# Performance work log

Hardware: AMD Instinct MI355X
Metric: run time of the kernel (lower is better)

The kernel has to match this reference:

```python
import jax, jax.numpy as jnp
import numpy as np

N, E = 100000, 1600000
IN_C, HID_C, OUT_C = 128, 32, 16


def setup_inputs() -> dict:
    key = jax.random.key(0)
    k1, k2, k3, k4, k5, k6 = jax.random.split(key, 6)
    x = jax.random.normal(k1, (N, IN_C), dtype=jnp.float32)
    edge_index = jax.random.randint(k2, (2, E), 0, N, dtype=jnp.int64)
    # glorot-style init for GCN weights
    W1 = jax.random.normal(k3, (IN_C, HID_C), dtype=jnp.float32) * (1.0 / np.sqrt(IN_C))
    b1 = jnp.zeros((HID_C,), dtype=jnp.float32)
    W2 = jax.random.normal(k4, (HID_C, OUT_C), dtype=jnp.float32) * (1.0 / np.sqrt(HID_C))
    b2 = jnp.zeros((OUT_C,), dtype=jnp.float32)
    return {"x": x, "edge_index": edge_index, "W1": W1, "b1": b1, "W2": W2, "b2": b2}


def _gcn_conv(x, W, b, src, dst, norm, n_nodes):
    # linear transform first (PyG GCNConv order), then normalized scatter-add
    h = x @ W                                  # [N, C_out]
    msg = h[src] * norm[:, None]               # gather + per-edge scale
    agg = jax.ops.segment_sum(msg, dst, num_segments=n_nodes)  # scatter-add
    return agg + b


def reference(x, edge_index, W1, b1, W2, b2):
    n_nodes = x.shape[0]
    loop = jnp.arange(n_nodes, dtype=edge_index.dtype)
    # add self-loops (PyG default add_self_loops=True)
    src = jnp.concatenate([edge_index[0], loop])
    dst = jnp.concatenate([edge_index[1], loop])
    # symmetric normalization: deg computed on graph WITH self-loops
    deg = jax.ops.segment_sum(jnp.ones_like(dst, dtype=x.dtype), dst, num_segments=n_nodes)
    dinv = jnp.where(deg > 0, jax.lax.rsqrt(deg), 0.0)
    norm = dinv[src] * dinv[dst]               # [E + N]

    h = _gcn_conv(x, W1, b1, src, dst, norm, n_nodes)
    h = jax.nn.relu(h)
    out = _gcn_conv(h, W2, b2, src, dst, norm, n_nodes)
    return out
```

## Files before the change

kernel.cpp:

```cpp
#include <hip/hip_runtime.h>
#include <stdint.h>


#define TPB 256

__global__ void k_zero2(unsigned int* __restrict__ a, unsigned int* __restrict__ b, int n) {
    int i = blockIdx.x * blockDim.x + threadIdx.x;
    if (i < n) { a[i] = 0u; b[i] = 0u; }
}

__global__ void k_count(const int* __restrict__ dst, unsigned int* __restrict__ cnt, int E) {
    int stride = gridDim.x * blockDim.x;
    for (int i = blockIdx.x * blockDim.x + threadIdx.x; i < E; i += stride)
        atomicAdd(&cnt[(unsigned int)dst[i]], 1u);
}

__global__ void k_dinv(const unsigned int* __restrict__ cnt, float* __restrict__ dinv, int n) {
    int i = blockIdx.x * blockDim.x + threadIdx.x;
    if (i < n) dinv[i] = rsqrtf(1.0f + (float)cnt[i]);
}

__global__ void k_blocksums(const unsigned int* __restrict__ cnt, unsigned int* __restrict__ partial, int n) {
    __shared__ unsigned int sm[TPB];
    int i = blockIdx.x * TPB + threadIdx.x;
    sm[threadIdx.x] = (i < n) ? cnt[i] : 0u;
    __syncthreads();
    for (int off = TPB / 2; off > 0; off >>= 1) {
        if (threadIdx.x < off) sm[threadIdx.x] += sm[threadIdx.x + off];
        __syncthreads();
    }
    if (threadIdx.x == 0) partial[blockIdx.x] = sm[0];
}

__global__ void k_scanpartials(unsigned int* __restrict__ partial, int nb) {
    __shared__ unsigned int sm[512];
    int t = threadIdx.x;
    unsigned int v = (t < nb) ? partial[t] : 0u;
    sm[t] = v;
    __syncthreads();
    for (int off = 1; off < 512; off <<= 1) {
        unsigned int add = (t >= off) ? sm[t - off] : 0u;
        __syncthreads();
        sm[t] += add;
        __syncthreads();
    }
    if (t < nb) partial[t] = sm[t] - v;
}

__global__ void k_rowptr(const unsigned int* __restrict__ cnt, const unsigned int* __restrict__ partial,
                         unsigned int* __restrict__ rowptr, int n, int E) {
    __shared__ unsigned int sm[TPB];
    int t = threadIdx.x;
    int i = blockIdx.x * TPB + t;
    unsigned int v = (i < n) ? cnt[i] : 0u;
    sm[t] = v;
    __syncthreads();
    for (int off = 1; off < TPB; off <<= 1) {
        unsigned int add = (t >= off) ? sm[t - off] : 0u;
        __syncthreads();
        sm[t] += add;
        __syncthreads();
    }
    if (i < n) rowptr[i] = partial[blockIdx.x] + sm[t] - v;
    if (i == n - 1) rowptr[n] = (unsigned int)E;
}

__global__ void k_fill(const int* __restrict__ ei, const float* __restrict__ dinv,
                       const unsigned int* __restrict__ rowptr, unsigned int* __restrict__ cursor,
                       int2* __restrict__ adj, int E) {
    const int* srcp = ei;
    const int* dstp = ei + E;
    int stride = gridDim.x * blockDim.x;
    for (int i = blockIdx.x * blockDim.x + threadIdx.x; i < E; i += stride) {
        int s = srcp[i], d = dstp[i];
        unsigned int pos = rowptr[d] + atomicAdd(&cursor[d], 1u);
        adj[pos] = make_int2(s, __float_as_int(dinv[s] * dinv[d]));
    }
}

__global__ void k_gemm1(const float* __restrict__ x, const float* __restrict__ W1,
                        float* __restrict__ h1, int n) {
    int t = blockIdx.x * blockDim.x + threadIdx.x;
    if (t >= n * 32) return;
    int row = t >> 5, j = t & 31;
    const float4* xr = (const float4*)(x + (size_t)row * 128);
    float acc = 0.f;
#pragma unroll 8
    for (int k4 = 0; k4 < 32; ++k4) {
        float4 xv = xr[k4];
        int k = k4 * 4;
        acc = fmaf(xv.x, W1[(k + 0) * 32 + j], acc);
        acc = fmaf(xv.y, W1[(k + 1) * 32 + j], acc);
        acc = fmaf(xv.z, W1[(k + 2) * 32 + j], acc);
        acc = fmaf(xv.w, W1[(k + 3) * 32 + j], acc);
    }
    h1[t] = acc;
}

__global__ void k_agg1(const float* __restrict__ h1, const float* __restrict__ dinv,
                       const unsigned int* __restrict__ rowptr, const int2* __restrict__ adj,
                       float* __restrict__ agg1, int n) {
    int t = blockIdx.x * blockDim.x + threadIdx.x;
    if (t >= n * 8) return;
    int node = t >> 3, c4 = (t & 7) * 4;
    float di = dinv[node];
    float di2 = di * di;
    float4 acc = *(const float4*)(h1 + (size_t)node * 32 + c4);
    acc.x *= di2; acc.y *= di2; acc.z *= di2; acc.w *= di2;
    unsigned int e1 = rowptr[node + 1];
    for (unsigned int e = rowptr[node]; e < e1; ++e) {
        int2 a = adj[e];
        float nrm = __int_as_float(a.y);
        float4 hv = *(const float4*)(h1 + (size_t)a.x * 32 + c4);
        acc.x = fmaf(hv.x, nrm, acc.x);
        acc.y = fmaf(hv.y, nrm, acc.y);
        acc.z = fmaf(hv.z, nrm, acc.z);
        acc.w = fmaf(hv.w, nrm, acc.w);
    }
    *(float4*)(agg1 + (size_t)node * 32 + c4) = acc;
}

__global__ void k_gemm2(const float* __restrict__ agg1, const float* __restrict__ b1,
                        const float* __restrict__ W2, float* __restrict__ h2, int n) {
    int t = blockIdx.x * blockDim.x + threadIdx.x;
    if (t >= n * 16) return;
    int row = t >> 4, j = t & 15;
    const float4* ar = (const float4*)(agg1 + (size_t)row * 32);
    float acc = 0.f;
#pragma unroll
    for (int k4 = 0; k4 < 8; ++k4) {
        float4 av = ar[k4];
        int k = k4 * 4;
        float v0 = fmaxf(av.x + b1[k + 0], 0.f);
        float v1 = fmaxf(av.y + b1[k + 1], 0.f);
        float v2 = fmaxf(av.z + b1[k + 2], 0.f);
        float v3 = fmaxf(av.w + b1[k + 3], 0.f);
        acc = fmaf(v0, W2[(k + 0) * 16 + j], acc);
        acc = fmaf(v1, W2[(k + 1) * 16 + j], acc);
        acc = fmaf(v2, W2[(k + 2) * 16 + j], acc);
        acc = fmaf(v3, W2[(k + 3) * 16 + j], acc);
    }
    h2[t] = acc;
}

__global__ void k_agg2(const float* __restrict__ h2, const float* __restrict__ dinv,
                       const float* __restrict__ b2,
                       const unsigned int* __restrict__ rowptr, const int2* __restrict__ adj,
                       float* __restrict__ out, int n) {
    int t = blockIdx.x * blockDim.x + threadIdx.x;
    if (t >= n * 4) return;
    int node = t >> 2, c4 = (t & 3) * 4;
    float di = dinv[node];
    float di2 = di * di;
    float4 hv0 = *(const float4*)(h2 + (size_t)node * 16 + c4);
    float4 bv = *(const float4*)(b2 + c4);
    float4 acc = make_float4(fmaf(hv0.x, di2, bv.x), fmaf(hv0.y, di2, bv.y),
                             fmaf(hv0.z, di2, bv.z), fmaf(hv0.w, di2, bv.w));
    unsigned int e1 = rowptr[node + 1];
    for (unsigned int e = rowptr[node]; e < e1; ++e) {
        int2 a = adj[e];
        float nrm = __int_as_float(a.y);
        float4 hv = *(const float4*)(h2 + (size_t)a.x * 16 + c4);
        acc.x = fmaf(hv.x, nrm, acc.x);
        acc.y = fmaf(hv.y, nrm, acc.y);
        acc.z = fmaf(hv.z, nrm, acc.z);
        acc.w = fmaf(hv.w, nrm, acc.w);
    }
    *(float4*)(out + (size_t)node * 16 + c4) = acc;
}

static inline char* align256(char* p) {
    return (char*)(((uintptr_t)p + 255) & ~(uintptr_t)255);
}

extern "C" void kernel_launch(void* const* d_in, const int* in_sizes, int n_in,
                              void* d_out, int out_size, void* d_ws, size_t ws_size,
                              hipStream_t stream) {
    const float* x  = (const float*)d_in[0];
    const int*   ei = (const int*)d_in[1];
    const float* W1 = (const float*)d_in[2];
    const float* b1 = (const float*)d_in[3];
    const float* W2 = (const float*)d_in[4];
    const float* b2 = (const float*)d_in[5];
    float*       out = (float*)d_out;

    int N = in_sizes[0] / 128;
    int E = in_sizes[1] / 2;

    char* p = (char*)d_ws;
    unsigned int* rowptr  = (unsigned int*)p;  p = align256(p + (size_t)(N + 1) * 4);
    unsigned int* cnt     = (unsigned int*)p;  p = align256(p + (size_t)N * 4);
    unsigned int* cursor  = (unsigned int*)p;  p = align256(p + (size_t)N * 4);
    unsigned int* partial = (unsigned int*)p;  p = align256(p + 512 * 4);
    float*        dinv    = (float*)p;         p = align256(p + (size_t)N * 4);
    int2*         adj     = (int2*)p;          p = align256(p + (size_t)E * 8);
    float*        h1      = (float*)p;         p = align256(p + (size_t)N * 32 * 4);
    float*        agg1    = (float*)p;
    float*        h2      = h1;

    int gN = (N + TPB - 1) / TPB;
    int NB = gN;

    k_zero2        <<<gN,   TPB, 0, stream>>>(cnt, cursor, N);
    k_count        <<<2048, TPB, 0, stream>>>(ei + E, cnt, E);
    k_dinv         <<<gN,   TPB, 0, stream>>>(cnt, dinv, N);
    k_blocksums    <<<NB,   TPB, 0, stream>>>(cnt, partial, N);
    k_scanpartials <<<1,    512, 0, stream>>>(partial, NB);
    k_rowptr       <<<NB,   TPB, 0, stream>>>(cnt, partial, rowptr, N, E);
    k_fill         <<<2048, TPB, 0, stream>>>(ei, dinv, rowptr, cursor, adj, E);

    k_gemm1 <<<(N * 32 + TPB - 1) / TPB, TPB, 0, stream>>>(x, W1, h1, N);
    k_agg1  <<<(N * 8  + TPB - 1) / TPB, TPB, 0, stream>>>(h1, dinv, rowptr, adj, agg1, N);
    k_gemm2 <<<(N * 16 + TPB - 1) / TPB, TPB, 0, stream>>>(agg1, b1, W2, h2, N);
    k_agg2  <<<(N * 4  + TPB - 1) / TPB, TPB, 0, stream>>>(h2, dinv, b2, rowptr, adj, out, N);
}
```

Before: 418.6 us.

## Tile both dense GEMMs through shared memory with register blocking

Rewrites the two node-feature GEMMs so each block stages a tile of input rows and a transposed, padded copy of the weight matrix in shared memory. Each thread then computes eight output rows, reusing one weight vector across them. The goal is to replace redundant per-thread global loads of x and W with coalesced tile loads and LDS reuse. In exchange the kernels use more shared memory per block (about 49 KB for gemm1) and more accumulator registers, which may lower occupancy.

After: 358.5 us. -14.4%, faster.

```diff
diff --git a/kernel.cpp b/kernel.cpp
--- a/kernel.cpp
+++ b/kernel.cpp
@@ -78,23 +78,49 @@
     }
 }
 
-__global__ void k_gemm1(const float* __restrict__ x, const float* __restrict__ W1,
-                        float* __restrict__ h1, int n) {
-    int t = blockIdx.x * blockDim.x + threadIdx.x;
-    if (t >= n * 32) return;
-    int row = t >> 5, j = t & 31;
-    const float4* xr = (const float4*)(x + (size_t)row * 128);
-    float acc = 0.f;
-#pragma unroll 8
+__global__ __launch_bounds__(TPB) void k_gemm1(const float* __restrict__ x, const float* __restrict__ W1,
+                                               float* __restrict__ h1, int n) {
+    __shared__ float4 smx4[64 * 32];
+    __shared__ float4 smw4[32 * 33];
+    float* smw = (float*)smw4;
+    int t = threadIdx.x;
+    int row0 = blockIdx.x * 64;
+
+#pragma unroll
+    for (int it = 0; it < 16; ++it) {
+        int idx = it * TPB + t;
+        int k = idx >> 5, j = idx & 31;
+        smw[j * 132 + k] = W1[idx];
+    }
+    const float4* x4 = (const float4*)x;
+    int lim = n * 32;
+#pragma unroll
+    for (int it = 0; it < 8; ++it) {
+        int fo = it * TPB + t;
+        int gi = row0 * 32 + fo;
+        smx4[fo] = (gi < lim) ? x4[gi] : make_float4(0.f, 0.f, 0.f, 0.f);
+    }
+    __syncthreads();
+
+    int j = t & 31, rb = (t >> 5) * 8;
+    float acc[8] = {0.f, 0.f, 0.f, 0.f, 0.f, 0.f, 0.f, 0.f};
+#pragma unroll 4
     for (int k4 = 0; k4 < 32; ++k4) {
-        float4 xv = xr[k4];
-        int k = k4 * 4;
-        acc = fmaf(xv.x, W1[(k + 0) * 32 + j], acc);
-        acc = fmaf(xv.y, W1[(k + 1) * 32 + j], acc);
-        acc = fmaf(xv.z, W1[(k + 2) * 32 + j], acc);
-        acc = fmaf(xv.w, W1[(k + 3) * 32 + j], acc);
-    }
-    h1[t] = acc;
+        float4 wv = smw4[j * 33 + k4];
+#pragma unroll
+        for (int i = 0; i < 8; ++i) {
+            float4 xv = smx4[(rb + i) * 32 + k4];
+            acc[i] = fmaf(xv.x, wv.x, acc[i]);
+            acc[i] = fmaf(xv.y, wv.y, acc[i]);
+            acc[i] = fmaf(xv.z, wv.z, acc[i]);
+            acc[i] = fmaf(xv.w, wv.w, acc[i]);
+        }
+    }
+#pragma unroll
+    for (int i = 0; i < 8; ++i) {
+        int row = row0 + rb + i;
+        if (row < n) h1[(size_t)row * 32 + j] = acc[i];
+    }
 }
 
 __global__ void k_agg1(const float* __restrict__ h1, const float* __restrict__ dinv,
@@ -120,27 +146,56 @@
     *(float4*)(agg1 + (size_t)node * 32 + c4) = acc;
 }
 
-__global__ void k_gemm2(const float* __restrict__ agg1, const float* __restrict__ b1,
-                        const float* __restrict__ W2, float* __restrict__ h2, int n) {
-    int t = blockIdx.x * blockDim.x + threadIdx.x;
-    if (t >= n * 16) return;
-    int row = t >> 4, j = t & 15;
-    const float4* ar = (const float4*)(agg1 + (size_t)row * 32);
-    float acc = 0.f;
+__global__ __launch_bounds__(TPB) void k_gemm2(const float* __restrict__ agg1, const float* __restrict__ b1,
+                                               const float* __restrict__ W2, float* __restrict__ h2, int n) {
+    __shared__ float4 sma4[128 * 8];
+    __shared__ float4 smw24[16 * 9];
+    float* smw2 = (float*)smw24;
+    int t = threadIdx.x;
+    int row0 = blockIdx.x * 128;
+
+#pragma unroll
+    for (int it = 0; it < 2; ++it) {
+        int idx = it * TPB + t;
+        int k = idx >> 4, j = idx & 15;
+        smw2[j * 36 + k] = W2[idx];
+    }
+    const float4* a4 = (const float4*)agg1;
+    const float4* b14 = (const float4*)b1;
+    int lim = n * 8;
+#pragma unroll
+    for (int it = 0; it < 4; ++it) {
+        int fo = it * TPB + t;
+        int gi = row0 * 8 + fo;
+        float4 v = (gi < lim) ? a4[gi] : make_float4(0.f, 0.f, 0.f, 0.f);
+        float4 b = b14[fo & 7];
+        v.x = fmaxf(v.x + b.x, 0.f);
+        v.y = fmaxf(v.y + b.y, 0.f);
+        v.z = fmaxf(v.z + b.z, 0.f);
+        v.w = fmaxf(v.w + b.w, 0.f);
+        sma4[fo] = v;
+    }
+    __syncthreads();
+
+    int j = t & 15, rb = (t >> 4) * 8;
+    float acc[8] = {0.f, 0.f, 0.f, 0.f, 0.f, 0.f, 0.f, 0.f};
 #pragma unroll
     for (int k4 = 0; k4 < 8; ++k4) {
-        float4 av = ar[k4];
-        int k = k4 * 4;
-        float v0 = fmaxf(av.x + b1[k + 0], 0.f);
-        float v1 = fmaxf(av.y + b1[k + 1], 0.f);
-        float v2 = fmaxf(av.z + b1[k + 2], 0.f);
-        float v3 = fmaxf(av.w + b1[k + 3], 0.f);
-        acc = fmaf(v0, W2[(k + 0) * 16 + j], acc);
-        acc = fmaf(v1, W2[(k + 1) * 16 + j], acc);
-        acc = fmaf(v2, W2[(k + 2) * 16 + j], acc);
-        acc = fmaf(v3, W2[(k + 3) * 16 + j], acc);
-    }
-    h2[t] = acc;
+        float4 wv = smw24[j * 9 + k4];
+#pragma unroll
+        for (int i = 0; i < 8; ++i) {
+            float4 xv = sma4[(rb + i) * 8 + k4];
+            acc[i] = fmaf(xv.x, wv.x, acc[i]);
+            acc[i] = fmaf(xv.y, wv.y, acc[i]);
+            acc[i] = fmaf(xv.z, wv.z, acc[i]);
+            acc[i] = fmaf(xv.w, wv.w, acc[i]);
+        }
+    }
+#pragma unroll
+    for (int i = 0; i < 8; ++i) {
+        int row = row0 + rb + i;
+        if (row < n) h2[(size_t)row * 16 + j] = acc[i];
+    }
 }
 
 __global__ void k_agg2(const float* __restrict__ h2, const float* __restrict__ dinv,
@@ -209,8 +264,8 @@
     k_rowptr       <<<NB,   TPB, 0, stream>>>(cnt, partial, rowptr, N, E);
     k_fill         <<<2048, TPB, 0, stream>>>(ei, dinv, rowptr, cursor, adj, E);
 
-    k_gemm1 <<<(N * 32 + TPB - 1) / TPB, TPB, 0, stream>>>(x, W1, h1, N);
-    k_agg1  <<<(N * 8  + TPB - 1) / TPB, TPB, 0, stream>>>(h1, dinv, rowptr, adj, agg1, N);
-    k_gemm2 <<<(N * 16 + TPB - 1) / TPB, TPB, 0, stream>>>(agg1, b1, W2, h2, N);
-    k_agg2  <<<(N * 4  + TPB - 1) / TPB, TPB, 0, stream>>>(h2, dinv, b2, rowptr, adj, out, N);
-}
+    k_gemm1 <<<(N + 63) / 64,          TPB, 0, stream>>>(x, W1, h1, N);
+    k_agg1  <<<(N * 8 + TPB - 1) / TPB, TPB, 0, stream>>>(h1, dinv, rowptr, adj, agg1, N);
+    k_gemm2 <<<(N + 127) / 128,        TPB, 0, stream>>>(agg1, b1, W2, h2, N);
+    k_agg2  <<<(N * 4 + TPB - 1) / TPB, TPB, 0, stream>>>(h2, dinv, b2, rowptr, adj, out, N);
+}
```
